# Performance work log

Hardware: AMD Instinct MI355X
Metric: run time of the kernel (lower is better)

## Reference

```python
import jax, jax.numpy as jnp
import numpy as np
from jax import lax

U, K, POOL, STRIDE, FC = 300, 19, 7, 7, 100   # num_units, filter size, maxpool, fc_size
B, L, D = 256, 1000, 4                        # batch, seq len, DNA dim
P = (L - (K - 1) - (POOL - 1) - 1) // STRIDE + 1  # post_pool_size = 140
EPS = 1e-5  # BatchNorm eps (eval mode with running stats; Dropout is identity in eval)


def setup_inputs() -> dict:
    key = jax.random.key(0)
    ks = jax.random.split(key, 24)
    rn = lambda k, shp, s=0.1: jax.random.normal(k, shp, jnp.float32) * s
    return {
        "input_seq": jax.random.normal(ks[0], (B, L, D), jnp.float32),
        # per-unit conv (groups=U on tiled input == plain Conv1d(4, U, K))
        "w_conv": rn(ks[1], (U, D, K)), "b_conv": rn(ks[2], (U,)),
        "g1": 1.0 + rn(ks[3], (U,)), "be1": rn(ks[4], (U,)),
        "m1": rn(ks[5], (U,)), "v1": 1.0 + jax.random.uniform(ks[6], (U,), jnp.float32),
        # per-unit FC1 (grouped 1x1 conv: P -> FC per unit)
        "w_fc1": rn(ks[7], (U, FC, P)), "b_fc1": rn(ks[8], (U, FC)),
        "g2": 1.0 + rn(ks[9], (U, FC)), "be2": rn(ks[10], (U, FC)),
        "m2": rn(ks[11], (U, FC)), "v2": 1.0 + jax.random.uniform(ks[12], (U, FC), jnp.float32),
        # per-unit FC2 (grouped 1x1 conv: FC -> 1 per unit)
        "w_fc2": rn(ks[13], (U, FC)), "b_fc2": rn(ks[14], (U,)),
        "g3": 1.0 + rn(ks[15], (U,)), "be3": rn(ks[16], (U,)),
        "m3": rn(ks[17], (U,)), "v3": 1.0 + jax.random.uniform(ks[18], (U,), jnp.float32),
        # final Linear(U, 1)
        "w_out": rn(ks[19], (U, 1)), "b_out": rn(ks[20], (1,)),
    }


def reference(input_seq, w_conv, b_conv, g1, be1, m1, v1, w_fc1, b_fc1,
              g2, be2, m2, v2, w_fc2, b_fc2, g3, be3, m3, v3, w_out, b_out):
    x = jnp.transpose(input_seq, (0, 2, 1))  # B,D,L
    # grouped conv on input tiled U times: every group sees the same D=4 channels,
    # so it is exactly a plain Conv1d(D, U, K).
    conv = lax.conv_general_dilated(
        x, w_conv, (1,), 'VALID', dimension_numbers=('NCH', 'OIH', 'NCH')
    ) + b_conv[None, :, None]                 # B,U,L' (L'=L-K+1)
    a = (conv - m1[None, :, None]) * (g1 / jnp.sqrt(v1 + EPS))[None, :, None] + be1[None, :, None]
    a = jnp.exp(a)
    pooled = lax.reduce_window(a, -jnp.inf, lax.max,
                               (1, 1, POOL), (1, 1, STRIDE), 'VALID')  # B,U,P
    # Flatten->Unsqueeze->grouped 1x1 conv == per-unit matmul over P
    h = jnp.einsum('bup,ufp->buf', pooled, w_fc1) + b_fc1               # B,U,FC
    h = jax.nn.relu((h - m2) * (g2 / jnp.sqrt(v2 + EPS)) + be2)
    z = jnp.einsum('buf,uf->bu', h, w_fc2) + b_fc2                      # B,U
    z = jax.nn.relu((z - m3) * (g3 / jnp.sqrt(v3 + EPS)) + be3)
    return jax.nn.sigmoid(z @ w_out + b_out)                            # B,1
```

## Files before the change

### kernel.cpp

```cpp
#include <hip/hip_runtime.h>
#include <hip/hip_bf16.h>
#include <math.h>

#define U_   300
#define K_   19
#define FC_  100
#define B_   256
#define L_   1000
#define P_   140
#define EPS_ 1e-5f
#define UP_  128
#define KP_  144

typedef unsigned short ushort_t;
typedef __attribute__((ext_vector_type(8)))  short short8v;
typedef __attribute__((ext_vector_type(16))) float f32x16;

__device__ __forceinline__ ushort_t f2bf(float f) {
    union { float f; unsigned u; } a; a.f = f;
    unsigned r = a.u + 0x7fffu + ((a.u >> 16) & 1u);
    return (ushort_t)(r >> 16);
}

__global__ __launch_bounds__(256, 4)
void pack_all_k(const float* __restrict__ w_conv, const float* __restrict__ b_conv,
                const float* __restrict__ g1, const float* __restrict__ be1,
                const float* __restrict__ m1, const float* __restrict__ v1,
                const float* __restrict__ w_fc1, const float* __restrict__ b_fc1,
                const float* __restrict__ g2, const float* __restrict__ be2,
                const float* __restrict__ m2, const float* __restrict__ v2,
                const float* __restrict__ w_fc2,
                ushort_t* __restrict__ w_bf, float* __restrict__ o1g,
                ushort_t* __restrict__ w1p, float* __restrict__ o2p,
                float* __restrict__ w2p)
{
    const int t = blockIdx.x * 256 + threadIdx.x;
    if (t < U_ * UP_ * KP_) {
        const int u = t / (UP_ * KP_);
        const int r = t - u * (UP_ * KP_);
        const int f = r / KP_;
        const int k = r - f * KP_;
        float val = 0.f;
        if (f < FC_ && k < P_) {
            const int fg = u * FC_ + f;
            const float s2 = g2[fg] / sqrtf(v2[fg] + EPS_);
            val = w_fc1[(size_t)fg * P_ + k] * s2;
        }
        w1p[t] = f2bf(val);
    }
    if (t < U_ * UP_) {
        const int u = t / UP_, f = t - u * UP_;
        float o2 = 0.f, w2 = 0.f;
        if (f < FC_) {
            const int fg = u * FC_ + f;
            const float s2 = g2[fg] / sqrtf(v2[fg] + EPS_);
            o2 = (b_fc1[fg] - m2[fg]) * s2 + be2[fg];
            w2 = w_fc2[fg];
        }
        o2p[t] = o2;
        w2p[t] = w2;
    }
    if (t < 320 * 80) {
        const int u = t / 80, j = t - u * 80;
        float val = 0.f;
        if (u < U_ && j < 76) {
            const int tp = j >> 2;
            const int d  = j & 3;
            const float s1 = g1[u] / sqrtf(v1[u] + EPS_);
            val = w_conv[u * 76 + 19 * d + tp] * s1;
        }
        w_bf[t] = f2bf(val);
    }
    if (t < 320) {
        float o = 0.f;
        if (t < U_) {
            const float s1 = g1[t] / sqrtf(v1[t] + EPS_);
            o = (b_conv[t] - m1[t]) * s1 + be1[t];
        }
        o1g[t] = o;
    }
}

__global__ __launch_bounds__(256, 4)
void conv_mfma_k(const float4* __restrict__ x4,
                 const ushort_t* __restrict__ w_bf,
                 const float* __restrict__ o1g,
                 ushort_t* __restrict__ pooled)
{
    __shared__ ushort_t xls[1000];
    const int tid = threadIdx.x;
    const int b   = blockIdx.y;
    const int bx  = blockIdx.x;
    const int w0  = bx * 32;
    const int l0  = w0 * 7;

    if (tid < 248) {
        const int gi = l0 + tid;
        float4 v = make_float4(0.f, 0.f, 0.f, 0.f);
        if (gi < L_) v = x4[(size_t)b * L_ + gi];
        ushort4 pk;
        pk.x = f2bf(v.x); pk.y = f2bf(v.y); pk.z = f2bf(v.z); pk.w = f2bf(v.w);
        *(ushort4*)&xls[4 * tid] = pk;
    }
    __syncthreads();

    const int lane = tid & 63;
    const int wv   = tid >> 6;
    const int half = lane >> 5;
    const int r32  = lane & 31;

    const int sreg = (r32 & 3) + 4 * (r32 >> 3);
    const int sh   = (r32 >> 2) & 1;
    const int off  = sreg < 7  ? sreg + 7 * sh
                   : sreg < 14 ? sreg + 7 + 7 * sh
                               : 28 + (sreg - 14) + 2 * sh;

    const char* xbA = (const char*)xls + 8 * (28 * (2 * wv)     + off) + 16 * half;
    const char* xbB = (const char*)xls + 8 * (28 * (2 * wv + 1) + off) + 16 * half;
    const char* wbase = (const char*)w_bf + 16 * half + 160 * r32;

    const int pA = w0 + 8 * wv;
    const int pB = pA + 4;

    for (int nt = 0; nt < 10; ++nt) {
        const int u = nt * 32 + r32;
        const float o1u = o1g[u];

        short8v bfr[5];
        const char* wb = wbase + nt * 5120;
#pragma unroll
        for (int kc = 0; kc < 5; ++kc)
            bfr[kc] = *(const short8v*)(wb + 32 * kc);

        f32x16 accA = {};
        f32x16 accB = {};
#pragma unroll
        for (int kc = 0; kc < 5; ++kc) {
            const short8v a0 = *(const short8v*)(xbA + 32 * kc);
            const short8v a1 = *(const short8v*)(xbB + 32 * kc);
            accA = __builtin_amdgcn_mfma_f32_32x32x16_bf16(a0, bfr[kc], accA, 0, 0, 0);
            accB = __builtin_amdgcn_mfma_f32_32x32x16_bf16(a1, bfr[kc], accB, 0, 0, 0);
        }

        float mA0 = accA[0], mA1 = accA[7];
        float mB0 = accB[0], mB1 = accB[7];
#pragma unroll
        for (int j = 1; j < 7; ++j) { mA0 = fmaxf(mA0, accA[j]); mB0 = fmaxf(mB0, accB[j]); }
#pragma unroll
        for (int j = 8; j < 14; ++j) { mA1 = fmaxf(mA1, accA[j]); mB1 = fmaxf(mB1, accB[j]); }

        const unsigned pkA = (unsigned)f2bf(__expf(mA0 + o1u)) |
                             ((unsigned)f2bf(__expf(mA1 + o1u)) << 16);
        const unsigned pkB = (unsigned)f2bf(__expf(mB0 + o1u)) |
                             ((unsigned)f2bf(__expf(mB1 + o1u)) << 16);
        const unsigned oA = __shfl_xor(pkA, 32);
        const unsigned oB = __shfl_xor(pkB, 32);

        if (u < U_) {
            if (half == 0) {
                if (pA + 3 < P_) {
                    ushort4 st;
                    st.x = (ushort_t)(pkA & 0xffff);
                    st.y = (ushort_t)(oA  & 0xffff);
                    st.z = (ushort_t)(pkA >> 16);
                    st.w = (ushort_t)(oA  >> 16);
                    *(ushort4*)&pooled[((size_t)u * B_ + b) * P_ + pA] = st;
                }
            } else {
                if (pB + 3 < P_) {
                    ushort4 st;
                    st.x = (ushort_t)(oB  & 0xffff);
                    st.y = (ushort_t)(pkB & 0xffff);
                    st.z = (ushort_t)(oB  >> 16);
                    st.w = (ushort_t)(pkB >> 16);
                    *(ushort4*)&pooled[((size_t)u * B_ + b) * P_ + pB] = st;
                }
            }
        }
    }
}

__global__ __launch_bounds__(256, 3)
void fc_mfma_k(const ushort_t* __restrict__ pooled,
               const ushort_t* __restrict__ w1p,
               const float* __restrict__ o2p,
               const float* __restrict__ w2p,
               const float* __restrict__ b_fc2,
               const float* __restrict__ g3,
               const float* __restrict__ be3,
               const float* __restrict__ m3,
               const float* __restrict__ v3,
               float* __restrict__ zbuf)
{
    __shared__ float zred[128][33];
    const int tid  = threadIdx.x;
    const int u    = blockIdx.y;
    const int bt   = blockIdx.x;
    const int lane = tid & 63;
    const int wv   = tid >> 6;
    const int half = lane >> 5;
    const int r32  = lane & 31;

    const int brow = bt * 128 + wv * 32 + r32;
    const ushort_t* __restrict__ abase =
        pooled + ((size_t)u * B_ + brow) * P_ + half * 8;
    const ushort_t* __restrict__ bbase =
        w1p + ((size_t)u * UP_ + r32) * KP_ + half * 8;

    f32x16 acc0 = {}, acc1 = {}, acc2 = {}, acc3 = {};
#pragma unroll
    for (int kc = 0; kc < 9; ++kc) {
        const short8v a  = *(const short8v*)(abase + kc * 16);
        const short8v b0 = *(const short8v*)(bbase            + kc * 16);
        const short8v b1 = *(const short8v*)(bbase + 32 * KP_ + kc * 16);
        const short8v b2 = *(const short8v*)(bbase + 64 * KP_ + kc * 16);
        const short8v b3 = *(const short8v*)(bbase + 96 * KP_ + kc * 16);
        acc0 = __builtin_amdgcn_mfma_f32_32x32x16_bf16(a, b0, acc0, 0, 0, 0);
        acc1 = __builtin_amdgcn_mfma_f32_32x32x16_bf16(a, b1, acc1, 0, 0, 0);
        acc2 = __builtin_amdgcn_mfma_f32_32x32x16_bf16(a, b2, acc2, 0, 0, 0);
        acc3 = __builtin_amdgcn_mfma_f32_32x32x16_bf16(a, b3, acc3, 0, 0, 0);
    }

    const int fb = u * UP_ + r32;
    const float o20 = o2p[fb],      w20 = w2p[fb];
    const float o21 = o2p[fb + 32], w21 = w2p[fb + 32];
    const float o22 = o2p[fb + 64], w22 = w2p[fb + 64];
    const float o23 = o2p[fb + 96], w23 = w2p[fb + 96];
#pragma unroll
    for (int rg = 0; rg < 16; ++rg) {
        const int row = (rg & 3) + 8 * (rg >> 2) + 4 * half;
        float s = fmaxf(acc0[rg] + o20, 0.f) * w20;
        s = fmaf(fmaxf(acc1[rg] + o21, 0.f), w21, s);
        s = fmaf(fmaxf(acc2[rg] + o22, 0.f), w22, s);
        s = fmaf(fmaxf(acc3[rg] + o23, 0.f), w23, s);
        zred[wv * 32 + row][r32] = s;
    }
    __syncthreads();

    if (tid < 128) {
        float s = 0.f;
#pragma unroll
        for (int j = 0; j < 32; ++j) s += zred[tid][j];
        const float s3 = g3[u] / sqrtf(v3[u] + EPS_);
        const float o3 = (b_fc2[u] - m3[u]) * s3 + be3[u];
        zbuf[(size_t)u * B_ + bt * 128 + tid] = fmaxf(fmaf(s, s3, o3), 0.f);
    }
}

__global__ __launch_bounds__(320, 2)
void out_k(const float* __restrict__ zbuf,
           const float* __restrict__ w_out,
           const float* __restrict__ b_out,
           float* __restrict__ out)
{
    __shared__ float red[5];
    const int tid = threadIdx.x;
    const int b   = blockIdx.x;

    float v = 0.f;
    if (tid < U_) v = zbuf[(size_t)tid * B_ + b] * w_out[tid];
#pragma unroll
    for (int o = 32; o > 0; o >>= 1) v += __shfl_xor(v, o);
    if ((tid & 63) == 0) red[tid >> 6] = v;
    __syncthreads();
    if (tid == 0) {
        const float s = red[0] + red[1] + red[2] + red[3] + red[4] + b_out[0];
        out[b] = 1.0f / (1.0f + __expf(-s));
    }
}

extern "C" void kernel_launch(void* const* d_in, const int* in_sizes, int n_in,
                              void* d_out, int out_size, void* d_ws, size_t ws_size,
                              hipStream_t stream)
{
    const float* input_seq = (const float*)d_in[0];
    const float* w_conv    = (const float*)d_in[1];
    const float* b_conv    = (const float*)d_in[2];
    const float* g1        = (const float*)d_in[3];
    const float* be1       = (const float*)d_in[4];
    const float* m1        = (const float*)d_in[5];
    const float* v1        = (const float*)d_in[6];
    const float* w_fc1     = (const float*)d_in[7];
    const float* b_fc1     = (const float*)d_in[8];
    const float* g2        = (const float*)d_in[9];
    const float* be2       = (const float*)d_in[10];
    const float* m2        = (const float*)d_in[11];
    const float* v2        = (const float*)d_in[12];
    const float* w_fc2     = (const float*)d_in[13];
    const float* b_fc2     = (const float*)d_in[14];
    const float* g3        = (const float*)d_in[15];
    const float* be3       = (const float*)d_in[16];
    const float* m3        = (const float*)d_in[17];
    const float* v3        = (const float*)d_in[18];
    const float* w_out     = (const float*)d_in[19];
    const float* b_out     = (const float*)d_in[20];

    char* p = (char*)d_ws;
    ushort_t* pooled = (ushort_t*)p;                 p += (size_t)B_ * U_ * P_ * 2;
    ushort_t* w1p    = (ushort_t*)p;                 p += (size_t)U_ * UP_ * KP_ * 2;
    float*    o2p    = (float*)p;                    p += (size_t)U_ * UP_ * 4;
    float*    w2p    = (float*)p;                    p += (size_t)U_ * UP_ * 4;
    ushort_t* w_bf   = (ushort_t*)p;                 p += 320 * 80 * 2;
    float*    o1g    = (float*)p;                    p += 320 * 4;
    float*    zbuf   = (float*)p;                    p += (size_t)U_ * B_ * 4;

    pack_all_k<<<dim3((U_ * UP_ * KP_ + 255) / 256), 256, 0, stream>>>(
        w_conv, b_conv, g1, be1, m1, v1,
        w_fc1, b_fc1, g2, be2, m2, v2, w_fc2,
        w_bf, o1g, w1p, o2p, w2p);

    conv_mfma_k<<<dim3(5, B_), 256, 0, stream>>>(
        (const float4*)input_seq, w_bf, o1g, pooled);

    fc_mfma_k<<<dim3(2, U_), 256, 0, stream>>>(
        pooled, w1p, o2p, w2p, b_fc2, g3, be3, m3, v3, zbuf);

    out_k<<<dim3(B_), 320, 0, stream>>>(zbuf, w_out, b_out, (float*)d_out);
}
```

Measured before the change: 65.00 us.

## Retile conv to skip padded pool outputs, prefetch MFMA operands, transpose z for output

The conv kernel now covers 28 pool outputs per block instead of 32, so the last wave's second tile is dropped rather than computed and discarded. The activation fragments are hoisted out of the unit loop, and the weight fragments for the next unit tile are prefetched while the current one runs. The FC kernel software-pipelines its operand loads one k-chunk ahead. z is now stored batch-major with padding, so the output kernel becomes a single-wave float4 dot product. Prefetching raises register pressure, and the conv launch-bounds hint drops from 4 to 2 blocks per SM, which may reduce occupancy.

Result: faster. 63.26 us (-2.7%).

```diff
diff --git a/kernel.cpp b/kernel.cpp
--- a/kernel.cpp
+++ b/kernel.cpp
@@ -81,20 +81,20 @@
     }
 }
 
-__global__ __launch_bounds__(256, 4)
+__global__ __launch_bounds__(256, 2)
 void conv_mfma_k(const float4* __restrict__ x4,
                  const ushort_t* __restrict__ w_bf,
                  const float* __restrict__ o1g,
                  ushort_t* __restrict__ pooled)
 {
-    __shared__ ushort_t xls[1000];
+    __shared__ ushort_t xls[880];
     const int tid = threadIdx.x;
     const int b   = blockIdx.y;
     const int bx  = blockIdx.x;
-    const int w0  = bx * 32;
+    const int w0  = bx * 28;
     const int l0  = w0 * 7;
 
-    if (tid < 248) {
+    if (tid < 220) {
         const int gi = l0 + tid;
         float4 v = make_float4(0.f, 0.f, 0.f, 0.f);
         if (gi < L_) v = x4[(size_t)b * L_ + gi];
@@ -108,6 +108,9 @@
     const int wv   = tid >> 6;
     const int half = lane >> 5;
     const int r32  = lane & 31;
+    const bool hasB = (wv < 3);
+    const int tA = 2 * wv;
+    const int tB = hasB ? (2 * wv + 1) : 0;
 
     const int sreg = (r32 & 3) + 4 * (r32 >> 3);
     const int sh   = (r32 >> 2) & 1;
@@ -115,68 +118,87 @@
                    : sreg < 14 ? sreg + 7 + 7 * sh
                                : 28 + (sreg - 14) + 2 * sh;
 
-    const char* xbA = (const char*)xls + 8 * (28 * (2 * wv)     + off) + 16 * half;
-    const char* xbB = (const char*)xls + 8 * (28 * (2 * wv + 1) + off) + 16 * half;
+    const char* xbA = (const char*)xls + 8 * (28 * tA + off) + 16 * half;
+    const char* xbB = (const char*)xls + 8 * (28 * tB + off) + 16 * half;
     const char* wbase = (const char*)w_bf + 16 * half + 160 * r32;
+
+    short8v aA[5], aB[5];
+#pragma unroll
+    for (int kc = 0; kc < 5; ++kc) {
+        aA[kc] = *(const short8v*)(xbA + 32 * kc);
+        aB[kc] = *(const short8v*)(xbB + 32 * kc);
+    }
 
     const int pA = w0 + 8 * wv;
     const int pB = pA + 4;
 
+    short8v bfr[5];
+#pragma unroll
+    for (int kc = 0; kc < 5; ++kc)
+        bfr[kc] = *(const short8v*)(wbase + 32 * kc);
+    float o1u = o1g[r32];
+
     for (int nt = 0; nt < 10; ++nt) {
-        const int u = nt * 32 + r32;
-        const float o1u = o1g[u];
-
-        short8v bfr[5];
-        const char* wb = wbase + nt * 5120;
+        const int ntn = (nt < 9) ? nt + 1 : nt;
+        short8v bnx[5];
+        const char* wn = wbase + ntn * 5120;
 #pragma unroll
         for (int kc = 0; kc < 5; ++kc)
-            bfr[kc] = *(const short8v*)(wb + 32 * kc);
+            bnx[kc] = *(const short8v*)(wn + 32 * kc);
+        const float o1n = o1g[ntn * 32 + r32];
 
         f32x16 accA = {};
+#pragma unroll
+        for (int kc = 0; kc < 5; ++kc)
+            accA = __builtin_amdgcn_mfma_f32_32x32x16_bf16(aA[kc], bfr[kc], accA, 0, 0, 0);
         f32x16 accB = {};
-#pragma unroll
-        for (int kc = 0; kc < 5; ++kc) {
-            const short8v a0 = *(const short8v*)(xbA + 32 * kc);
-            const short8v a1 = *(const short8v*)(xbB + 32 * kc);
-            accA = __builtin_amdgcn_mfma_f32_32x32x16_bf16(a0, bfr[kc], accA, 0, 0, 0);
-            accB = __builtin_amdgcn_mfma_f32_32x32x16_bf16(a1, bfr[kc], accB, 0, 0, 0);
+        if (hasB) {
+#pragma unroll
+            for (int kc = 0; kc < 5; ++kc)
+                accB = __builtin_amdgcn_mfma_f32_32x32x16_bf16(aB[kc], bfr[kc], accB, 0, 0, 0);
         }
 
         float mA0 = accA[0], mA1 = accA[7];
-        float mB0 = accB[0], mB1 = accB[7];
-#pragma unroll
-        for (int j = 1; j < 7; ++j) { mA0 = fmaxf(mA0, accA[j]); mB0 = fmaxf(mB0, accB[j]); }
-#pragma unroll
-        for (int j = 8; j < 14; ++j) { mA1 = fmaxf(mA1, accA[j]); mB1 = fmaxf(mB1, accB[j]); }
-
+#pragma unroll
+        for (int j = 1; j < 7; ++j)  mA0 = fmaxf(mA0, accA[j]);
+#pragma unroll
+        for (int j = 8; j < 14; ++j) mA1 = fmaxf(mA1, accA[j]);
         const unsigned pkA = (unsigned)f2bf(__expf(mA0 + o1u)) |
                              ((unsigned)f2bf(__expf(mA1 + o1u)) << 16);
-        const unsigned pkB = (unsigned)f2bf(__expf(mB0 + o1u)) |
-                             ((unsigned)f2bf(__expf(mB1 + o1u)) << 16);
         const unsigned oA = __shfl_xor(pkA, 32);
-        const unsigned oB = __shfl_xor(pkB, 32);
-
-        if (u < U_) {
-            if (half == 0) {
-                if (pA + 3 < P_) {
-                    ushort4 st;
-                    st.x = (ushort_t)(pkA & 0xffff);
-                    st.y = (ushort_t)(oA  & 0xffff);
-                    st.z = (ushort_t)(pkA >> 16);
-                    st.w = (ushort_t)(oA  >> 16);
-                    *(ushort4*)&pooled[((size_t)u * B_ + b) * P_ + pA] = st;
-                }
-            } else {
-                if (pB + 3 < P_) {
-                    ushort4 st;
-                    st.x = (ushort_t)(oB  & 0xffff);
-                    st.y = (ushort_t)(pkB & 0xffff);
-                    st.z = (ushort_t)(oB  >> 16);
-                    st.w = (ushort_t)(pkB >> 16);
-                    *(ushort4*)&pooled[((size_t)u * B_ + b) * P_ + pB] = st;
-                }
+
+        const int u = nt * 32 + r32;
+        if (u < U_ && half == 0) {
+            ushort4 st;
+            st.x = (ushort_t)(pkA & 0xffff);
+            st.y = (ushort_t)(oA  & 0xffff);
+            st.z = (ushort_t)(pkA >> 16);
+            st.w = (ushort_t)(oA  >> 16);
+            *(ushort4*)&pooled[((size_t)u * B_ + b) * P_ + pA] = st;
+        }
+
+        if (hasB) {
+            float mB0 = accB[0], mB1 = accB[7];
+#pragma unroll
+            for (int j = 1; j < 7; ++j)  mB0 = fmaxf(mB0, accB[j]);
+#pragma unroll
+            for (int j = 8; j < 14; ++j) mB1 = fmaxf(mB1, accB[j]);
+            const unsigned pkB = (unsigned)f2bf(__expf(mB0 + o1u)) |
+                                 ((unsigned)f2bf(__expf(mB1 + o1u)) << 16);
+            const unsigned oB = __shfl_xor(pkB, 32);
+            if (u < U_ && half == 1) {
+                ushort4 st;
+                st.x = (ushort_t)(oB  & 0xffff);
+                st.y = (ushort_t)(pkB & 0xffff);
+                st.z = (ushort_t)(oB  >> 16);
+                st.w = (ushort_t)(pkB >> 16);
+                *(ushort4*)&pooled[((size_t)u * B_ + b) * P_ + pB] = st;
             }
         }
+
+#pragma unroll
+        for (int kc = 0; kc < 5; ++kc) bfr[kc] = bnx[kc];
+        o1u = o1n;
     }
 }
 
@@ -190,7 +212,7 @@
                const float* __restrict__ be3,
                const float* __restrict__ m3,
                const float* __restrict__ v3,
-               float* __restrict__ zbuf)
+               float* __restrict__ zT)
 {
     __shared__ float zred[128][33];
     const int tid  = threadIdx.x;
@@ -207,18 +229,26 @@
     const ushort_t* __restrict__ bbase =
         w1p + ((size_t)u * UP_ + r32) * KP_ + half * 8;
 
+    short8v ac  = *(const short8v*)(abase);
+    short8v b0c = *(const short8v*)(bbase);
+    short8v b1c = *(const short8v*)(bbase + 32 * KP_);
+    short8v b2c = *(const short8v*)(bbase + 64 * KP_);
+    short8v b3c = *(const short8v*)(bbase + 96 * KP_);
+
     f32x16 acc0 = {}, acc1 = {}, acc2 = {}, acc3 = {};
 #pragma unroll
     for (int kc = 0; kc < 9; ++kc) {
-        const short8v a  = *(const short8v*)(abase + kc * 16);
-        const short8v b0 = *(const short8v*)(bbase            + kc * 16);
-        const short8v b1 = *(const short8v*)(bbase + 32 * KP_ + kc * 16);
-        const short8v b2 = *(const short8v*)(bbase + 64 * KP_ + kc * 16);
-        const short8v b3 = *(const short8v*)(bbase + 96 * KP_ + kc * 16);
-        acc0 = __builtin_amdgcn_mfma_f32_32x32x16_bf16(a, b0, acc0, 0, 0, 0);
-        acc1 = __builtin_amdgcn_mfma_f32_32x32x16_bf16(a, b1, acc1, 0, 0, 0);
-        acc2 = __builtin_amdgcn_mfma_f32_32x32x16_bf16(a, b2, acc2, 0, 0, 0);
-        acc3 = __builtin_amdgcn_mfma_f32_32x32x16_bf16(a, b3, acc3, 0, 0, 0);
+        const int kn = (kc < 8) ? kc + 1 : kc;
+        const short8v an  = *(const short8v*)(abase + kn * 16);
+        const short8v b0n = *(const short8v*)(bbase            + kn * 16);
+        const short8v b1n = *(const short8v*)(bbase + 32 * KP_ + kn * 16);
+        const short8v b2n = *(const short8v*)(bbase + 64 * KP_ + kn * 16);
+        const short8v b3n = *(const short8v*)(bbase + 96 * KP_ + kn * 16);
+        acc0 = __builtin_amdgcn_mfma_f32_32x32x16_bf16(ac, b0c, acc0, 0, 0, 0);
+        acc1 = __builtin_amdgcn_mfma_f32_32x32x16_bf16(ac, b1c, acc1, 0, 0, 0);
+        acc2 = __builtin_amdgcn_mfma_f32_32x32x16_bf16(ac, b2c, acc2, 0, 0, 0);
+        acc3 = __builtin_amdgcn_mfma_f32_32x32x16_bf16(ac, b3c, acc3, 0, 0, 0);
+        ac = an; b0c = b0n; b1c = b1n; b2c = b2n; b3c = b3n;
     }
 
     const int fb = u * UP_ + r32;
@@ -243,30 +273,30 @@
         for (int j = 0; j < 32; ++j) s += zred[tid][j];
         const float s3 = g3[u] / sqrtf(v3[u] + EPS_);
         const float o3 = (b_fc2[u] - m3[u]) * s3 + be3[u];
-        zbuf[(size_t)u * B_ + bt * 128 + tid] = fmaxf(fmaf(s, s3, o3), 0.f);
-    }
-}
-
-__global__ __launch_bounds__(320, 2)
-void out_k(const float* __restrict__ zbuf,
+        zT[(size_t)(bt * 128 + tid) * 304 + u] = fmaxf(fmaf(s, s3, o3), 0.f);
+    }
+}
+
+__global__ __launch_bounds__(64, 8)
+void out_k(const float* __restrict__ zT,
            const float* __restrict__ w_out,
            const float* __restrict__ b_out,
            float* __restrict__ out)
 {
-    __shared__ float red[5];
-    const int tid = threadIdx.x;
-    const int b   = blockIdx.x;
-
-    float v = 0.f;
-    if (tid < U_) v = zbuf[(size_t)tid * B_ + b] * w_out[tid];
-#pragma unroll
-    for (int o = 32; o > 0; o >>= 1) v += __shfl_xor(v, o);
-    if ((tid & 63) == 0) red[tid >> 6] = v;
-    __syncthreads();
-    if (tid == 0) {
-        const float s = red[0] + red[1] + red[2] + red[3] + red[4] + b_out[0];
-        out[b] = 1.0f / (1.0f + __expf(-s));
-    }
+    const int lane = threadIdx.x;
+    const int b    = blockIdx.x;
+    const float4* zr = (const float4*)(zT + (size_t)b * 304);
+    const float4* w4 = (const float4*)w_out;
+
+    float s = 0.f;
+    for (int i = lane; i < 75; i += 64) {
+        const float4 z = zr[i], w = w4[i];
+        s += z.x * w.x + z.y * w.y + z.z * w.z + z.w * w.w;
+    }
+#pragma unroll
+    for (int o = 32; o > 0; o >>= 1) s += __shfl_xor(s, o);
+    if (lane == 0)
+        out[b] = 1.0f / (1.0f + __expf(-(s + b_out[0])));
 }
 
 extern "C" void kernel_launch(void* const* d_in, const int* in_sizes, int n_in,
@@ -302,7 +332,7 @@
     float*    w2p    = (float*)p;                    p += (size_t)U_ * UP_ * 4;
     ushort_t* w_bf   = (ushort_t*)p;                 p += 320 * 80 * 2;
     float*    o1g    = (float*)p;                    p += 320 * 4;
-    float*    zbuf   = (float*)p;                    p += (size_t)U_ * B_ * 4;
+    float*    zT     = (float*)p;                    p += (size_t)B_ * 304 * 4;
 
     pack_all_k<<<dim3((U_ * UP_ * KP_ + 255) / 256), 256, 0, stream>>>(
         w_conv, b_conv, g1, be1, m1, v1,
@@ -313,7 +343,7 @@
         (const float4*)input_seq, w_bf, o1g, pooled);
 
     fc_mfma_k<<<dim3(2, U_), 256, 0, stream>>>(
-        pooled, w1p, o2p, w2p, b_fc2, g3, be3, m3, v3, zbuf);
-
-    out_k<<<dim3(B_), 320, 0, stream>>>(zbuf, w_out, b_out, (float*)d_out);
-}
+        pooled, w1p, o2p, w2p, b_fc2, g3, be3, m3, v3, zT);
+
+    out_k<<<dim3(B_), 64, 0, stream>>>(zT, w_out, b_out, (float*)d_out);
+}
```
